# Performance work log

Hardware: AMD Instinct MI355X
Metric: run time of the kernel (lower is better)

Reference implementation:

```python
import jax, jax.numpy as jnp
import numpy as np

B, T, C, H = 2, 2048, 1024, 16
HD = C // H  # head dim = 64


def setup_inputs() -> dict:
    key = jax.random.key(0)
    ks = jax.random.split(key, 9)
    s = 1.0 / np.sqrt(C)
    return {
        "x": jax.random.normal(ks[0], (B, T, C), dtype=jnp.float32),
        "Wq": jax.random.normal(ks[1], (C, C), dtype=jnp.float32) * s,
        "bq": jax.random.normal(ks[2], (C,), dtype=jnp.float32) * 0.02,
        "Wk": jax.random.normal(ks[3], (C, C), dtype=jnp.float32) * s,
        "bk": jax.random.normal(ks[4], (C,), dtype=jnp.float32) * 0.02,
        "Wv": jax.random.normal(ks[5], (C, C), dtype=jnp.float32) * s,
        "bv": jax.random.normal(ks[6], (C,), dtype=jnp.float32) * 0.02,
        "Wo": jax.random.normal(ks[7], (C, C), dtype=jnp.float32) * s,
        "bo": jax.random.normal(ks[8], (C,), dtype=jnp.float32) * 0.02,
    }


def reference(x, Wq, bq, Wk, bk, Wv, bv, Wo, bo):
    # Projections (torch Linear: x @ W.T + b; here W stored pre-transposed as [C_in, C_out])
    q = x @ Wq + bq  # (B,T,C)
    k = x @ Wk + bk
    v = x @ Wv + bv
    # Split heads: (B,T,C) -> (B,H,T,HD)
    q = q.reshape(B, T, H, HD).transpose(0, 2, 1, 3)
    k = k.reshape(B, T, H, HD).transpose(0, 2, 1, 3)
    v = v.reshape(B, T, H, HD).transpose(0, 2, 1, 3)
    # NOTE: original module never applies a causal mask despite its name.
    score = jnp.einsum("bhqd,bhkd->bhqk", q, k) / jnp.sqrt(jnp.float32(HD))
    score = jax.nn.softmax(score, axis=-1)
    y = jnp.einsum("bhqk,bhkd->bhqd", score, v)
    y = y.transpose(0, 2, 1, 3).reshape(B, T, C)
    # dropout is identity in eval mode
    return y @ Wo + bo
```

## Files before the change

### kernel.cpp

```cpp
#include <hip/hip_runtime.h>
#include <math.h>

#define B_ 2
#define T_ 2048
#define C_ 1024
#define H_ 16
#define HD_ 64
#define M_ (B_*T_)

typedef _Float16 half2v __attribute__((ext_vector_type(2)));
typedef _Float16 half4v __attribute__((ext_vector_type(4)));
typedef _Float16 half8v __attribute__((ext_vector_type(8)));
typedef float f32x4 __attribute__((ext_vector_type(4)));

#define GLD_LDS(gp, lp) \
  __builtin_amdgcn_global_load_lds( \
      (const __attribute__((address_space(1))) void*)(gp), \
      (__attribute__((address_space(3))) void*)(lp), 16, 0, 0)

__global__ __launch_bounds__(256) void prep_kernel(
    const float* __restrict__ x,
    const float* __restrict__ Wq, const float* __restrict__ Wk,
    const float* __restrict__ Wv, const float* __restrict__ Wo,
    const float* __restrict__ bq, const float* __restrict__ bk,
    const float* __restrict__ bv,
    _Float16* __restrict__ xh, _Float16* __restrict__ Wt3,
    _Float16* __restrict__ Wot, float* __restrict__ b3)
{
  __shared__ float tile[32][33];
  const int blk = blockIdx.x, thr = threadIdx.x;
  if (blk < 4096) {
    int i = blk * 256 + thr;
    float4 v = ((const float4*)x)[i];
    half4v h; h[0] = (_Float16)v.x; h[1] = (_Float16)v.y;
    h[2] = (_Float16)v.z; h[3] = (_Float16)v.w;
    ((half4v*)xh)[i] = h;
  } else if (blk < 8192) {
    int zz = (blk - 4096) >> 10;
    int bxy = (blk - 4096) & 1023;
    const float* W; _Float16* Wt;
    switch (zz) {
      case 0:  W = Wq; Wt = Wt3; break;
      case 1:  W = Wk; Wt = Wt3 + (size_t)1024 * 1024; break;
      case 2:  W = Wv; Wt = Wt3 + (size_t)2048 * 1024; break;
      default: W = Wo; Wt = Wot; break;
    }
    const int n0 = (bxy & 31) * 32, k0 = (bxy >> 5) * 32;
    const int tx = thr & 31, ty = thr >> 5;
#pragma unroll
    for (int r = 0; r < 4; r++) {
      int k = ty + r * 8;
      tile[k][tx] = W[(size_t)(k0 + k) * C_ + n0 + tx];
    }
    __syncthreads();
#pragma unroll
    for (int r = 0; r < 4; r++) {
      int n = ty + r * 8;
      Wt[(size_t)(n0 + n) * C_ + k0 + tx] = (_Float16)tile[tx][n];
    }
  } else {
    int i = (blk - 8192) * 256 + thr;
    const float* s = (i < 1024) ? bq : ((i < 2048) ? bk : bv);
    b3[i] = s[i & 1023];
  }
}

template <int BM, int BN, int EPI>
__global__ __launch_bounds__(256) void gemm_f16_kernel(
    const _Float16* __restrict__ A, const _Float16* __restrict__ Bw,
    const float* __restrict__ bias,
    _Float16* __restrict__ o0, _Float16* __restrict__ o1,
    _Float16* __restrict__ o2, float* __restrict__ of)
{
  constexpr int FM = BM / 32, FN = BN / 32;
  __shared__ __align__(16) _Float16 As[BM * 32];
  __shared__ __align__(16) _Float16 Bs[BN * 32];
  const int t = threadIdx.x;
  const int w = t >> 6, lane = t & 63, l15 = lane & 15, quad = lane >> 4;
  const int wm = (w & 1) * (BM / 2), wn = (w >> 1) * (BN / 2);
  const int bm = blockIdx.y * BM, bn = blockIdx.x * BN;
  const int lrow = lane >> 2, lcol = (lane & 3) * 8;

  f32x4 acc[FM][FN];
#pragma unroll
  for (int i = 0; i < FM; i++)
#pragma unroll
    for (int j = 0; j < FN; j++) acc[i][j] = (f32x4){0.f, 0.f, 0.f, 0.f};

  for (int k0 = 0; k0 < 1024; k0 += 32) {
#pragma unroll
    for (int i = 0; i < BM / 64; i++) {
      int ca = w + 4 * i;
      int row = ca * 16 + lrow;
      GLD_LDS(A + (size_t)(bm + row) * 1024 + k0 + lcol, As + ca * 512);
    }
#pragma unroll
    for (int i = 0; i < BN / 64; i++) {
      int cb = w + 4 * i;
      int row = cb * 16 + lrow;
      GLD_LDS(Bw + (size_t)(bn + row) * 1024 + k0 + lcol, Bs + cb * 512);
    }
    __syncthreads();

    half8v af[FM], bf[FN];
#pragma unroll
    for (int mt = 0; mt < FM; mt++)
      af[mt] = *(const half8v*)(As + (wm + mt * 16 + l15) * 32 + quad * 8);
#pragma unroll
    for (int nt = 0; nt < FN; nt++)
      bf[nt] = *(const half8v*)(Bs + (wn + nt * 16 + l15) * 32 + quad * 8);
#pragma unroll
    for (int mt = 0; mt < FM; mt++)
#pragma unroll
      for (int nt = 0; nt < FN; nt++)
        acc[mt][nt] = __builtin_amdgcn_mfma_f32_16x16x32_f16(
            af[mt], bf[nt], acc[mt][nt], 0, 0, 0);
    __syncthreads();
  }

#pragma unroll
  for (int mt = 0; mt < FM; mt++)
#pragma unroll
    for (int nt = 0; nt < FN; nt++) {
      int n = bn + wn + nt * 16 + l15;
      float bv = bias[n];
      if (EPI == 0 && bn >= 2048) {
        int dg = n - 2048;
        int hh = dg >> 6, hd = dg & 63;
        int m0 = bm + wm + mt * 16 + quad * 4;
        int bb = m0 >> 11, tt = m0 & 2047;
        half2v p01 = __builtin_bit_cast(half2v,
            __builtin_amdgcn_cvt_pkrtz(acc[mt][nt][0] + bv, acc[mt][nt][1] + bv));
        half2v p23 = __builtin_bit_cast(half2v,
            __builtin_amdgcn_cvt_pkrtz(acc[mt][nt][2] + bv, acc[mt][nt][3] + bv));
        half4v pk = __builtin_shufflevector(p01, p23, 0, 1, 2, 3);
        *(half4v*)(o2 + (((size_t)(bb * H_ + hh) * 64 + hd) * 2048 + tt)) = pk;
      } else {
#pragma unroll
        for (int r = 0; r < 4; r++) {
          int m = bm + wm + mt * 16 + quad * 4 + r;
          float v = acc[mt][nt][r] + bv;
          if (EPI == 0) {
            if (bn < 1024) {
              o0[(size_t)m * 1024 + n] = (_Float16)(v * 0.180336884f);
            } else {
              o1[(size_t)m * 1024 + (n - 1024)] = (_Float16)v;
            }
          } else {
            of[(size_t)m * 1024 + n] = v;
          }
        }
      }
    }
}

__global__ __launch_bounds__(256) void attn_f16_kernel(
    const _Float16* __restrict__ Qh, const _Float16* __restrict__ Kh,
    const _Float16* __restrict__ Vt, _Float16* __restrict__ Yh)
{
  __shared__ __align__(16) _Float16 Ks[128 * 68];
  __shared__ __align__(16) _Float16 Vs[64 * 132];
  const int t = threadIdx.x;
  const int w = t >> 6, lane = t & 63, l15 = lane & 15, quad = lane >> 4;
  const int qt = blockIdx.x, h = blockIdx.y, b = blockIdx.z;
  const int qg = qt * 64 + w * 16 + l15;
  const size_t qoff = ((size_t)(b * T_ + qg)) * C_ + h * HD_;

  half8v qf[2];
  qf[0] = *(const half8v*)(Qh + qoff + quad * 8);
  qf[1] = *(const half8v*)(Qh + qoff + 32 + quad * 8);

  f32x4 o[4];
#pragma unroll
  for (int i = 0; i < 4; i++) o[i] = (f32x4){0.f, 0.f, 0.f, 0.f};
  float m_run = -INFINITY, l_run = 0.f;

  const size_t kbase = ((size_t)b * T_) * C_ + h * HD_;
  const size_t vbase = ((size_t)(b * H_ + h)) * HD_ * 2048;

  for (int kt0 = 0; kt0 < T_; kt0 += 128) {
#pragma unroll
    for (int i = 0; i < 4; i++) {
      int slot = t + i * 256;
      int row = slot >> 3, cp = slot & 7;
      *(uint4*)((char*)Ks + row * 136 + cp * 16) =
          *(const uint4*)(Kh + kbase + (size_t)(kt0 + row) * C_ + cp * 8);
    }
#pragma unroll
    for (int i = 0; i < 4; i++) {
      int slot = t + i * 256;
      int row = slot >> 4, cp = slot & 15;
      *(uint4*)((char*)Vs + row * 264 + cp * 16) =
          *(const uint4*)(Vt + vbase + (size_t)row * 2048 + kt0 + cp * 8);
    }
    __syncthreads();

    f32x4 s[8];
#pragma unroll
    for (int kt = 0; kt < 8; kt++) {
      s[kt] = (f32x4){0.f, 0.f, 0.f, 0.f};
      int key = kt * 16 + l15;
#pragma unroll
      for (int ks = 0; ks < 2; ks++) {
        half8v kf = *(const half8v*)((char*)Ks + key * 136 + (ks * 4 + quad) * 16);
        s[kt] = __builtin_amdgcn_mfma_f32_16x16x32_f16(kf, qf[ks], s[kt], 0, 0, 0);
      }
    }

    float tmax = -INFINITY;
#pragma unroll
    for (int kt = 0; kt < 8; kt++)
#pragma unroll
      for (int r = 0; r < 4; r++) tmax = fmaxf(tmax, s[kt][r]);
    tmax = fmaxf(tmax, __shfl_xor(tmax, 16));
    tmax = fmaxf(tmax, __shfl_xor(tmax, 32));
    float mnew = fmaxf(m_run, tmax);
    float alpha = __builtin_amdgcn_exp2f(m_run - mnew);

    float psum = 0.f;
    half4v pf[8];
#pragma unroll
    for (int kt = 0; kt < 8; kt++) {
      float p0 = __builtin_amdgcn_exp2f(s[kt][0] - mnew);
      float p1 = __builtin_amdgcn_exp2f(s[kt][1] - mnew);
      float p2 = __builtin_amdgcn_exp2f(s[kt][2] - mnew);
      float p3 = __builtin_amdgcn_exp2f(s[kt][3] - mnew);
      psum += (p0 + p1) + (p2 + p3);
      half2v pk01 = __builtin_bit_cast(half2v, __builtin_amdgcn_cvt_pkrtz(p0, p1));
      half2v pk23 = __builtin_bit_cast(half2v, __builtin_amdgcn_cvt_pkrtz(p2, p3));
      pf[kt] = __builtin_shufflevector(pk01, pk23, 0, 1, 2, 3);
    }
    psum += __shfl_xor(psum, 16);
    psum += __shfl_xor(psum, 32);
    l_run = l_run * alpha + psum;
    m_run = mnew;
#pragma unroll
    for (int dt = 0; dt < 4; dt++) o[dt] *= alpha;

#pragma unroll
    for (int dt = 0; dt < 4; dt++) {
      int d = dt * 16 + l15;
#pragma unroll
      for (int kt = 0; kt < 8; kt++) {
        half4v vf = *(const half4v*)((char*)Vs + d * 264 + kt * 32 + quad * 8);
        o[dt] = __builtin_amdgcn_mfma_f32_16x16x16f16(vf, pf[kt], o[dt], 0, 0, 0);
      }
    }
    __syncthreads();
  }

  float inv = 1.0f / l_run;
#pragma unroll
  for (int dt = 0; dt < 4; dt++) {
    half4v yv;
#pragma unroll
    for (int r = 0; r < 4; r++) yv[r] = (_Float16)(o[dt][r] * inv);
    *(half4v*)(Yh + qoff + dt * 16 + quad * 4) = yv;
  }
}

extern "C" void kernel_launch(void* const* d_in, const int* in_sizes, int n_in,
                              void* d_out, int out_size, void* d_ws, size_t ws_size,
                              hipStream_t stream) {
  const float* x  = (const float*)d_in[0];
  const float* Wq = (const float*)d_in[1];
  const float* bq = (const float*)d_in[2];
  const float* Wk = (const float*)d_in[3];
  const float* bk = (const float*)d_in[4];
  const float* Wv = (const float*)d_in[5];
  const float* bv = (const float*)d_in[6];
  const float* Wo = (const float*)d_in[7];
  const float* bo = (const float*)d_in[8];
  float* out = (float*)d_out;

  char* ws = (char*)d_ws;
  _Float16* xh   = (_Float16*)(ws);
  _Float16* Qh   = (_Float16*)(ws + (((size_t)8)  << 20));
  _Float16* Kh   = (_Float16*)(ws + (((size_t)16) << 20));
  _Float16* Vt   = (_Float16*)(ws + (((size_t)24) << 20));
  _Float16* Yh   = (_Float16*)(ws + (((size_t)32) << 20));
  _Float16* Wt3  = (_Float16*)(ws + (((size_t)40) << 20));
  _Float16* Wot  = (_Float16*)(ws + (((size_t)46) << 20));
  float*    b3   = (float*)   (ws + (((size_t)48) << 20));

  prep_kernel<<<8204, 256, 0, stream>>>(x, Wq, Wk, Wv, Wo, bq, bk, bv,
                                        xh, Wt3, Wot, b3);

  gemm_f16_kernel<128, 128, 0><<<dim3(24, 32), 256, 0, stream>>>(
      xh, Wt3, b3, Qh, Kh, Vt, nullptr);

  attn_f16_kernel<<<dim3(T_ / 64, H_, B_), 256, 0, stream>>>(Qh, Kh, Vt, Yh);

  gemm_f16_kernel<64, 128, 1><<<dim3(8, 64), 256, 0, stream>>>(
      Yh, Wot, bo, nullptr, nullptr, nullptr, out);
}
```

Baseline: 219.7 us.

## Split attention key range in two with partial outputs and merge kernel

```diff
diff --git a/kernel.cpp b/kernel.cpp
--- a/kernel.cpp
+++ b/kernel.cpp
@@ -156,13 +156,15 @@
 
 __global__ __launch_bounds__(256) void attn_f16_kernel(
     const _Float16* __restrict__ Qh, const _Float16* __restrict__ Kh,
-    const _Float16* __restrict__ Vt, _Float16* __restrict__ Yh)
+    const _Float16* __restrict__ Vt, _Float16* __restrict__ part0,
+    _Float16* __restrict__ part1, float* __restrict__ ml)
 {
-  __shared__ __align__(16) _Float16 Ks[128 * 68];
-  __shared__ __align__(16) _Float16 Vs[64 * 132];
+  __shared__ __align__(16) _Float16 Ks[64 * 68];
+  __shared__ __align__(16) _Float16 Vs[64 * 68];
   const int t = threadIdx.x;
   const int w = t >> 6, lane = t & 63, l15 = lane & 15, quad = lane >> 4;
-  const int qt = blockIdx.x, h = blockIdx.y, b = blockIdx.z;
+  const int qt = blockIdx.x, h = blockIdx.y;
+  const int b = blockIdx.z >> 1, half = blockIdx.z & 1;
   const int qg = qt * 64 + w * 16 + l15;
   const size_t qoff = ((size_t)(b * T_ + qg)) * C_ + h * HD_;
 
@@ -178,26 +180,24 @@
   const size_t kbase = ((size_t)b * T_) * C_ + h * HD_;
   const size_t vbase = ((size_t)(b * H_ + h)) * HD_ * 2048;
 
-  for (int kt0 = 0; kt0 < T_; kt0 += 128) {
-#pragma unroll
-    for (int i = 0; i < 4; i++) {
-      int slot = t + i * 256;
-      int row = slot >> 3, cp = slot & 7;
-      *(uint4*)((char*)Ks + row * 136 + cp * 16) =
-          *(const uint4*)(Kh + kbase + (size_t)(kt0 + row) * C_ + cp * 8);
-    }
-#pragma unroll
-    for (int i = 0; i < 4; i++) {
-      int slot = t + i * 256;
-      int row = slot >> 4, cp = slot & 15;
-      *(uint4*)((char*)Vs + row * 264 + cp * 16) =
-          *(const uint4*)(Vt + vbase + (size_t)row * 2048 + kt0 + cp * 8);
-    }
-    __syncthreads();
-
-    f32x4 s[8];
-#pragma unroll
-    for (int kt = 0; kt < 8; kt++) {
+  const int srow = t >> 3, scp = t & 7;
+  const int k0g = half * 1024;
+
+  for (int kt0 = 0; kt0 < 1024; kt0 += 64) {
+    const int kg = k0g + kt0;
+#pragma unroll
+    for (int i = 0; i < 2; i++) {
+      int row = srow + i * 32;
+      *(uint4*)((char*)Ks + row * 136 + scp * 16) =
+          *(const uint4*)(Kh + kbase + (size_t)(kg + row) * C_ + scp * 8);
+      *(uint4*)((char*)Vs + row * 136 + scp * 16) =
+          *(const uint4*)(Vt + vbase + (size_t)row * 2048 + kg + scp * 8);
+    }
+    __syncthreads();
+
+    f32x4 s[4];
+#pragma unroll
+    for (int kt = 0; kt < 4; kt++) {
       s[kt] = (f32x4){0.f, 0.f, 0.f, 0.f};
       int key = kt * 16 + l15;
 #pragma unroll
@@ -209,7 +209,7 @@
 
     float tmax = -INFINITY;
 #pragma unroll
-    for (int kt = 0; kt < 8; kt++)
+    for (int kt = 0; kt < 4; kt++)
 #pragma unroll
       for (int r = 0; r < 4; r++) tmax = fmaxf(tmax, s[kt][r]);
     tmax = fmaxf(tmax, __shfl_xor(tmax, 16));
@@ -218,9 +218,9 @@
     float alpha = __builtin_amdgcn_exp2f(m_run - mnew);
 
     float psum = 0.f;
-    half4v pf[8];
-#pragma unroll
-    for (int kt = 0; kt < 8; kt++) {
+    half4v pf[4];
+#pragma unroll
+    for (int kt = 0; kt < 4; kt++) {
       float p0 = __builtin_amdgcn_exp2f(s[kt][0] - mnew);
       float p1 = __builtin_amdgcn_exp2f(s[kt][1] - mnew);
       float p2 = __builtin_amdgcn_exp2f(s[kt][2] - mnew);
@@ -241,8 +241,8 @@
     for (int dt = 0; dt < 4; dt++) {
       int d = dt * 16 + l15;
 #pragma unroll
-      for (int kt = 0; kt < 8; kt++) {
-        half4v vf = *(const half4v*)((char*)Vs + d * 264 + kt * 32 + quad * 8);
+      for (int kt = 0; kt < 4; kt++) {
+        half4v vf = *(const half4v*)((char*)Vs + d * 136 + kt * 32 + quad * 8);
         o[dt] = __builtin_amdgcn_mfma_f32_16x16x16f16(vf, pf[kt], o[dt], 0, 0, 0);
       }
     }
@@ -250,13 +250,52 @@
   }
 
   float inv = 1.0f / l_run;
+  _Float16* pp = half ? part1 : part0;
+  const int q = w * 16 + l15;
+  const size_t pbase = ((((size_t)(b * H_ + h)) * 32 + qt) * 64 + q) * 64;
 #pragma unroll
   for (int dt = 0; dt < 4; dt++) {
     half4v yv;
 #pragma unroll
     for (int r = 0; r < 4; r++) yv[r] = (_Float16)(o[dt][r] * inv);
-    *(half4v*)(Yh + qoff + dt * 16 + quad * 4) = yv;
-  }
+    *(half4v*)(pp + pbase + dt * 16 + quad * 4) = yv;
+  }
+  if (quad == 0) {
+    size_t mlb = (size_t)half * 131072 +
+                 ((((size_t)(b * H_ + h)) * 32 + qt) * 64 + q) * 2;
+    ml[mlb] = m_run; ml[mlb + 1] = l_run;
+  }
+}
+
+__global__ __launch_bounds__(256) void attn_merge_kernel(
+    const _Float16* __restrict__ part0, const _Float16* __restrict__ part1,
+    const float* __restrict__ ml, _Float16* __restrict__ Yh)
+{
+  const int qt = blockIdx.x, h = blockIdx.y, b = blockIdx.z;
+  const int t = threadIdx.x;
+  const int q = t >> 2, dc = (t & 3) * 16;
+  const size_t rowi = (((size_t)(b * H_ + h)) * 32 + qt) * 64 + q;
+  const size_t pbase = rowi * 64 + dc;
+  float m0 = ml[rowi * 2], l0 = ml[rowi * 2 + 1];
+  float m1 = ml[131072 + rowi * 2], l1 = ml[131072 + rowi * 2 + 1];
+  float m = fmaxf(m0, m1);
+  float a0 = __builtin_amdgcn_exp2f(m0 - m) * l0;
+  float a1 = __builtin_amdgcn_exp2f(m1 - m) * l1;
+  float inv = 1.0f / (a0 + a1);
+  float w0 = a0 * inv, w1 = a1 * inv;
+  half8v x0a = *(const half8v*)(part0 + pbase);
+  half8v x0b = *(const half8v*)(part0 + pbase + 8);
+  half8v x1a = *(const half8v*)(part1 + pbase);
+  half8v x1b = *(const half8v*)(part1 + pbase + 8);
+  half8v ya, yb;
+#pragma unroll
+  for (int j = 0; j < 8; j++) {
+    ya[j] = (_Float16)(w0 * (float)x0a[j] + w1 * (float)x1a[j]);
+    yb[j] = (_Float16)(w0 * (float)x0b[j] + w1 * (float)x1b[j]);
+  }
+  _Float16* yp = Yh + ((size_t)(b * T_ + qt * 64 + q)) * C_ + h * HD_ + dc;
+  *(half8v*)yp = ya;
+  *(half8v*)(yp + 8) = yb;
 }
 
 extern "C" void kernel_launch(void* const* d_in, const int* in_sizes, int n_in,
@@ -274,14 +313,17 @@
   float* out = (float*)d_out;
 
   char* ws = (char*)d_ws;
-  _Float16* xh   = (_Float16*)(ws);
-  _Float16* Qh   = (_Float16*)(ws + (((size_t)8)  << 20));
-  _Float16* Kh   = (_Float16*)(ws + (((size_t)16) << 20));
-  _Float16* Vt   = (_Float16*)(ws + (((size_t)24) << 20));
-  _Float16* Yh   = (_Float16*)(ws + (((size_t)32) << 20));
-  _Float16* Wt3  = (_Float16*)(ws + (((size_t)40) << 20));
-  _Float16* Wot  = (_Float16*)(ws + (((size_t)46) << 20));
-  float*    b3   = (float*)   (ws + (((size_t)48) << 20));
+  _Float16* xh    = (_Float16*)(ws);
+  _Float16* Qh    = (_Float16*)(ws + (((size_t)8)  << 20));
+  _Float16* Kh    = (_Float16*)(ws + (((size_t)16) << 20));
+  _Float16* Vt    = (_Float16*)(ws + (((size_t)24) << 20));
+  _Float16* part0 = (_Float16*)(ws + (((size_t)32) << 20));
+  _Float16* part1 = xh;
+  _Float16* Ym    = Kh;
+  _Float16* Wt3   = (_Float16*)(ws + (((size_t)40) << 20));
+  _Float16* Wot   = (_Float16*)(ws + (((size_t)46) << 20));
+  float*    b3    = (float*)   (ws + (((size_t)48) << 20));
+  float*    ml    = (float*)   (ws + (((size_t)48) << 20) + 65536);
 
   prep_kernel<<<8204, 256, 0, stream>>>(x, Wq, Wk, Wv, Wo, bq, bk, bv,
                                         xh, Wt3, Wot, b3);
@@ -289,8 +331,10 @@
   gemm_f16_kernel<128, 128, 0><<<dim3(24, 32), 256, 0, stream>>>(
       xh, Wt3, b3, Qh, Kh, Vt, nullptr);
 
-  attn_f16_kernel<<<dim3(T_ / 64, H_, B_), 256, 0, stream>>>(Qh, Kh, Vt, Yh);
+  attn_f16_kernel<<<dim3(32, 16, 4), 256, 0, stream>>>(
+      Qh, Kh, Vt, part0, part1, ml);
+  attn_merge_kernel<<<dim3(32, 16, 2), 256, 0, stream>>>(part0, part1, ml, Ym);
 
   gemm_f16_kernel<64, 128, 1><<<dim3(8, 64), 256, 0, stream>>>(
-      Yh, Wot, bo, nullptr, nullptr, nullptr, out);
-}
+      Ym, Wot, bo, nullptr, nullptr, nullptr, out);
+}
```

After: 234.9 us. +6.9%, slower.
